# Kernel tuning notes

Hardware: AMD Instinct MI355X
Metric: run time of the kernel (lower is better)

## Reference

```python
import jax, jax.numpy as jnp
import numpy as np

N_LAYERS = 6
N_HEADS = 16
D_EMBED = 1024
D_HEAD = D_EMBED // N_HEADS
VOCAB = 32000
EXP = 4
B, S = 2, 1024


def setup_inputs() -> dict:
    key = jax.random.key(0)
    ks = jax.random.split(key, 24)
    f = jax.random.normal
    inp = {
        "input_ids": jax.random.randint(ks[0], (B, S), 0, VOCAB),
        "encoder_k": f(ks[1], (B, S, D_EMBED), jnp.float32),
        "encoder_v": f(ks[2], (B, S, D_EMBED), jnp.float32),
        "emb": f(ks[3], (VOCAB, D_EMBED), jnp.float32) * 0.02,
        # per-head projection weights (shared across heads), one per layer,
        # for masked self-attn (m) and cross-attn (c). stored as [L, d_head, d_head]
        # applied as x @ W (equivalent param'n of nn.Linear, bias=False)
        "Wq_m": f(ks[4], (N_LAYERS, D_HEAD, D_HEAD), jnp.float32) / np.sqrt(D_HEAD),
        "Wk_m": f(ks[5], (N_LAYERS, D_HEAD, D_HEAD), jnp.float32) / np.sqrt(D_HEAD),
        "Wv_m": f(ks[6], (N_LAYERS, D_HEAD, D_HEAD), jnp.float32) / np.sqrt(D_HEAD),
        "Wq_c": f(ks[7], (N_LAYERS, D_HEAD, D_HEAD), jnp.float32) / np.sqrt(D_HEAD),
        "Wk_c": f(ks[8], (N_LAYERS, D_HEAD, D_HEAD), jnp.float32) / np.sqrt(D_HEAD),
        "Wv_c": f(ks[9], (N_LAYERS, D_HEAD, D_HEAD), jnp.float32) / np.sqrt(D_HEAD),
        "ln1_g": jnp.ones((N_LAYERS, D_EMBED), jnp.float32),
        "ln1_b": jnp.zeros((N_LAYERS, D_EMBED), jnp.float32),
        "ln2_g": jnp.ones((N_LAYERS, D_EMBED), jnp.float32),
        "ln2_b": jnp.zeros((N_LAYERS, D_EMBED), jnp.float32),
        "ln3_g": jnp.ones((N_LAYERS, D_EMBED), jnp.float32),
        "ln3_b": jnp.zeros((N_LAYERS, D_EMBED), jnp.float32),
        "W1": f(ks[10], (N_LAYERS, D_EMBED, EXP * D_EMBED), jnp.float32) / np.sqrt(D_EMBED),
        "b1": jnp.zeros((N_LAYERS, EXP * D_EMBED), jnp.float32),
        "W2": f(ks[11], (N_LAYERS, EXP * D_EMBED, D_EMBED), jnp.float32) / np.sqrt(EXP * D_EMBED),
        "b2": jnp.zeros((N_LAYERS, D_EMBED), jnp.float32),
        "Wout": f(ks[12], (D_EMBED, VOCAB), jnp.float32) / np.sqrt(D_EMBED),
        "bout": jnp.zeros((VOCAB,), jnp.float32),
    }
    return inp


def _layer_norm(x, g, b, eps=1e-5):
    mu = jnp.mean(x, axis=-1, keepdims=True)
    var = jnp.var(x, axis=-1, keepdims=True)
    return (x - mu) * jax.lax.rsqrt(var + eps) * g + b


def _mha(k_in, q_in, v_in, Wk, Wq, Wv, causal_mask):
    b, s, _ = k_in.shape
    # split heads: [b, s, h, d_head]; per-head Linear shared across heads
    k = jnp.einsum("bshd,de->bshe", k_in.reshape(b, s, N_HEADS, D_HEAD), Wk)
    q = jnp.einsum("bshd,de->bshe", q_in.reshape(b, s, N_HEADS, D_HEAD), Wq)
    v = jnp.einsum("bshd,de->bshe", v_in.reshape(b, s, N_HEADS, D_HEAD), Wv)
    scores = jnp.einsum("bqhd,bkhd->bhqk", q, k) / np.sqrt(D_HEAD)
    if causal_mask is not None:
        # quirk of original: masked positions filled with 1e-19 (not -inf)
        scores = jnp.where(causal_mask, scores, jnp.asarray(1e-19, scores.dtype))
    attn = jax.nn.softmax(scores, axis=-1)
    out = jnp.einsum("bhqk,bkhd->bqhd", attn, v)
    return out.reshape(b, s, D_EMBED)


def _pos_encoding(s, d):
    # angle = pos / 10000 ** (2*i / d); sin if i even else cos (faithful quirk)
    pos = jnp.arange(s, dtype=jnp.float32)[:, None]
    i = jnp.arange(d, dtype=jnp.float32)[None, :]
    angle = pos / jnp.power(10000.0, 2.0 * i / d)
    return jnp.where(jnp.arange(d)[None, :] % 2 == 0, jnp.sin(angle), jnp.cos(angle))


def reference(input_ids, encoder_k, encoder_v, emb, Wq_m, Wk_m, Wv_m, Wq_c, Wk_c, Wv_c,
              ln1_g, ln1_b, ln2_g, ln2_b, ln3_g, ln3_b, W1, b1, W2, b2, Wout, bout):
    b, s = input_ids.shape
    causal = jnp.tril(jnp.ones((s, s), bool))[None, None]  # [1,1,s,s]
    x = emb[input_ids] * np.sqrt(D_EMBED) + _pos_encoding(s, D_EMBED)[None]
    for l in range(N_LAYERS):
        op = _mha(x, x, x, Wk_m[l], Wq_m[l], Wv_m[l], causal)
        h1 = _layer_norm(op + x, ln1_g[l], ln1_b[l])
        op = _mha(encoder_k, h1, encoder_v, Wk_c[l], Wq_c[l], Wv_c[l], None)
        h2 = _layer_norm(op + h1, ln2_g[l], ln2_b[l])
        ff = jax.nn.relu(h2 @ W1[l] + b1[l]) @ W2[l] + b2[l]
        x = _layer_norm(ff + h2, ln3_g[l], ln3_b[l])
    return x @ Wout + bout
```

## Files before the change

kernel.cpp:

```cpp
#include <hip/hip_runtime.h>
#include <math.h>

#define NB   2
#define SEQ  1024
#define TOK  2048
#define DEM  1024
#define NH   16
#define DH   64
#define FFD  4096
#define NL   6
#define VOC  32000

typedef __bf16 bf16x8 __attribute__((ext_vector_type(8)));
typedef float  f32x4  __attribute__((ext_vector_type(4)));
typedef const __attribute__((address_space(1))) void gvoid_t;
typedef __attribute__((address_space(3)))       void lvoid_t;

__device__ __forceinline__ int swz8(int r, int c8) {
  return r * 64 + (((c8 >> 3) ^ (r & 7)) << 3);
}

__global__ __launch_bounds__(256) void k_embed(const int* __restrict__ ids,
    const float* __restrict__ emb, float* __restrict__ x)
{
  int t = blockIdx.x;
  int s = t & (SEQ - 1);
  int id = ids[t];
  int d0 = threadIdx.x * 4;
  const float ln10000 = 9.210340371976184f;
  #pragma unroll
  for (int j = 0; j < 4; j++) {
    int i = d0 + j;
    float inv = expf(-(2.0f * (float)i / (float)DEM) * ln10000);
    float ang = (float)s * inv;
    float pe = ((i & 1) == 0) ? sinf(ang) : cosf(ang);
    x[(size_t)t * DEM + i] = emb[(size_t)id * DEM + i] * 32.0f + pe;
  }
}

__global__ __launch_bounds__(256) void k_proj3(
    const float* __restrict__ qi, const float* __restrict__ ki,
    const float* __restrict__ vi,
    const float* __restrict__ Wq, const float* __restrict__ Wk,
    const float* __restrict__ Wv,
    __bf16* __restrict__ qh, __bf16* __restrict__ ql_,
    __bf16* __restrict__ kh, __bf16* __restrict__ kl_,
    __bf16* __restrict__ vt)
{
  __shared__ float Ws[64][64];
  __shared__ float xs[64][68];
  int t0 = blockIdx.x * 64, hh = blockIdx.y, tid = threadIdx.x;
  const float* ins[3]  = {qi, ki, vi};
  const float* Wp[3]   = {Wq, Wk, Wv};
  #pragma unroll 1
  for (int p = 0; p < 3; p++) {
    if (p) __syncthreads();
    #pragma unroll
    for (int i = 0; i < 16; i++) {
      int idx = tid + i * 256;
      int r = idx >> 6, c = idx & 63;
      Ws[r][c] = Wp[p][idx];
      xs[c][r] = ins[p][(size_t)(t0 + r) * DEM + hh * DH + c];
    }
    __syncthreads();
    int e = tid & 63, tq = tid >> 6;
    float acc[16] = {0.f};
    for (int d = 0; d < 64; d++) {
      float w = Ws[d][e];
      float4 x0 = *(float4*)&xs[d][tq * 16 + 0];
      float4 x1 = *(float4*)&xs[d][tq * 16 + 4];
      float4 x2 = *(float4*)&xs[d][tq * 16 + 8];
      float4 x3 = *(float4*)&xs[d][tq * 16 + 12];
      acc[0]  += x0.x * w; acc[1]  += x0.y * w; acc[2]  += x0.z * w; acc[3]  += x0.w * w;
      acc[4]  += x1.x * w; acc[5]  += x1.y * w; acc[6]  += x1.z * w; acc[7]  += x1.w * w;
      acc[8]  += x2.x * w; acc[9]  += x2.y * w; acc[10] += x2.z * w; acc[11] += x2.w * w;
      acc[12] += x3.x * w; acc[13] += x3.y * w; acc[14] += x3.z * w; acc[15] += x3.w * w;
    }
    if (p == 2) {
      alignas(16) __bf16 tmp[16];
      #pragma unroll
      for (int i = 0; i < 16; i++) tmp[i] = (__bf16)acc[i];
      uint4* dst = (uint4*)&vt[(size_t)(hh * DH + e) * TOK + t0 + tq * 16];
      dst[0] = ((uint4*)tmp)[0];
      dst[1] = ((uint4*)tmp)[1];
    } else {
      __bf16* ho = p ? kh : qh;
      __bf16* lo = p ? kl_ : ql_;
      #pragma unroll
      for (int i = 0; i < 16; i++) {
        float v = acc[i];
        __bf16 hv = (__bf16)v;
        size_t idx = (size_t)(t0 + tq * 16 + i) * DEM + hh * DH + e;
        ho[idx] = hv;
        lo[idx] = (__bf16)(v - (float)hv);
      }
    }
  }
}

__global__ __launch_bounds__(256) void k_attn_mfma(
    const __bf16* __restrict__ qh, const __bf16* __restrict__ ql,
    const __bf16* __restrict__ kh, const __bf16* __restrict__ kl,
    const __bf16* __restrict__ vt, float* __restrict__ out, int causal)
{
  __shared__ __bf16 khs[64 * 64];
  __shared__ __bf16 kls[64 * 64];
  __shared__ __bf16 vts[64 * 64];
  __shared__ __bf16 phs[4][16 * 64];
  __shared__ __bf16 pls[4][16 * 64];

  int lin = (blockIdx.z * gridDim.y + blockIdx.y) * gridDim.x + blockIdx.x;
  int lin2 = (lin & 7) * 64 + (lin >> 3);
  int qt = lin2 & 15, h = (lin2 >> 4) & 15, b = lin2 >> 8;

  int tid = threadIdx.x, lane = tid & 63, w = tid >> 6;
  int fr = lane & 15, fkg = lane >> 4;
  int q0 = qt * 64;

  const __bf16* qhb = qh + ((size_t)(b * SEQ + q0 + w * 16 + fr)) * DEM + h * DH;
  const __bf16* qlb = ql + ((size_t)(b * SEQ + q0 + w * 16 + fr)) * DEM + h * DH;
  bf16x8 qf0 = *(const bf16x8*)(qhb + fkg * 8);
  bf16x8 qf1 = *(const bf16x8*)(qhb + fkg * 8 + 32);
  bf16x8 qg0 = *(const bf16x8*)(qlb + fkg * 8);
  bf16x8 qg1 = *(const bf16x8*)(qlb + fkg * 8 + 32);

  const __bf16* khb = kh + ((size_t)b * SEQ) * DEM + h * DH;
  const __bf16* klb = kl + ((size_t)b * SEQ) * DEM + h * DH;
  const __bf16* vtb = vt + (size_t)(h * DH) * TOK + b * SEQ;

  float m[4], l[4] = {0.f, 0.f, 0.f, 0.f};
  m[0] = m[1] = m[2] = m[3] = -INFINITY;
  f32x4 o[4] = {};
  int qrow_g = q0 + w * 16;

  for (int kt = 0; kt < 16; kt++) {
    if (kt) __syncthreads();
    #pragma unroll
    for (int i = 0; i < 2; i++) {
      int cid = tid + i * 256;
      int r = cid >> 3, cc = cid & 7;
      int sc = ((cc ^ (r & 7)) << 3);
      __builtin_amdgcn_global_load_lds(
          (gvoid_t*)(khb + (size_t)(kt * 64 + r) * DEM + sc),
          (lvoid_t*)(khs + cid * 8), 16, 0, 0);
      __builtin_amdgcn_global_load_lds(
          (gvoid_t*)(klb + (size_t)(kt * 64 + r) * DEM + sc),
          (lvoid_t*)(kls + cid * 8), 16, 0, 0);
      __builtin_amdgcn_global_load_lds(
          (gvoid_t*)(vtb + (size_t)r * TOK + kt * 64 + sc),
          (lvoid_t*)(vts + cid * 8), 16, 0, 0);
    }
    __syncthreads();

    f32x4 s[4] = {};
    #pragma unroll
    for (int j = 0; j < 4; j++) {
      int r0 = j * 16 + fr;
      bf16x8 a0 = *(const bf16x8*)(khs + swz8(r0, fkg * 8));
      bf16x8 a1 = *(const bf16x8*)(khs + swz8(r0, fkg * 8 + 32));
      bf16x8 b0 = *(const bf16x8*)(kls + swz8(r0, fkg * 8));
      bf16x8 b1 = *(const bf16x8*)(kls + swz8(r0, fkg * 8 + 32));
      s[j] = __builtin_amdgcn_mfma_f32_16x16x32_bf16(qf0, a0, s[j], 0, 0, 0);
      s[j] = __builtin_amdgcn_mfma_f32_16x16x32_bf16(qf1, a1, s[j], 0, 0, 0);
      s[j] = __builtin_amdgcn_mfma_f32_16x16x32_bf16(qf0, b0, s[j], 0, 0, 0);
      s[j] = __builtin_amdgcn_mfma_f32_16x16x32_bf16(qf1, b1, s[j], 0, 0, 0);
      s[j] = __builtin_amdgcn_mfma_f32_16x16x32_bf16(qg0, a0, s[j], 0, 0, 0);
      s[j] = __builtin_amdgcn_mfma_f32_16x16x32_bf16(qg1, a1, s[j], 0, 0, 0);
    }

    #pragma unroll
    for (int r = 0; r < 4; r++) {
      int qg = qrow_g + fkg * 4 + r;
      float sv[4];
      #pragma unroll
      for (int j = 0; j < 4; j++) {
        float x = s[j][r] * 0.125f;
        int kg = kt * 64 + j * 16 + fr;
        if (causal && kg > qg) x = 1e-19f;
        sv[j] = x;
      }
      float tmax = fmaxf(fmaxf(sv[0], sv[1]), fmaxf(sv[2], sv[3]));
      tmax = fmaxf(tmax, __shfl_xor(tmax, 1));
      tmax = fmaxf(tmax, __shfl_xor(tmax, 2));
      tmax = fmaxf(tmax, __shfl_xor(tmax, 4));
      tmax = fmaxf(tmax, __shfl_xor(tmax, 8));
      float mnew = fmaxf(m[r], tmax);
      float alpha = __expf(m[r] - mnew);
      float p0 = __expf(sv[0] - mnew), p1 = __expf(sv[1] - mnew);
      float p2 = __expf(sv[2] - mnew), p3 = __expf(sv[3] - mnew);
      float rs = p0 + p1 + p2 + p3;
      rs += __shfl_xor(rs, 1); rs += __shfl_xor(rs, 2);
      rs += __shfl_xor(rs, 4); rs += __shfl_xor(rs, 8);
      l[r] = l[r] * alpha + rs;
      m[r] = mnew;
      #pragma unroll
      for (int jd = 0; jd < 4; jd++) o[jd][r] *= alpha;
      int prow = fkg * 4 + r;
      float pv[4] = {p0, p1, p2, p3};
      #pragma unroll
      for (int j = 0; j < 4; j++) {
        int pcol = j * 16 + fr;
        int idx = prow * 64 + (((((pcol >> 3) ^ (prow & 7)) << 3)) | (pcol & 7));
        __bf16 hv = (__bf16)pv[j];
        phs[w][idx] = hv;
        pls[w][idx] = (__bf16)(pv[j] - (float)hv);
      }
    }

    bf16x8 pa0 = *(const bf16x8*)(&phs[w][swz8(fr, fkg * 8)]);
    bf16x8 pa1 = *(const bf16x8*)(&phs[w][swz8(fr, fkg * 8 + 32)]);
    bf16x8 pb0 = *(const bf16x8*)(&pls[w][swz8(fr, fkg * 8)]);
    bf16x8 pb1 = *(const bf16x8*)(&pls[w][swz8(fr, fkg * 8 + 32)]);
    #pragma unroll
    for (int jd = 0; jd < 4; jd++) {
      int vr0 = jd * 16 + fr;
      bf16x8 v0 = *(const bf16x8*)(vts + swz8(vr0, fkg * 8));
      bf16x8 v1 = *(const bf16x8*)(vts + swz8(vr0, fkg * 8 + 32));
      o[jd] = __builtin_amdgcn_mfma_f32_16x16x32_bf16(pa0, v0, o[jd], 0, 0, 0);
      o[jd] = __builtin_amdgcn_mfma_f32_16x16x32_bf16(pa1, v1, o[jd], 0, 0, 0);
      o[jd] = __builtin_amdgcn_mfma_f32_16x16x32_bf16(pb0, v0, o[jd], 0, 0, 0);
      o[jd] = __builtin_amdgcn_mfma_f32_16x16x32_bf16(pb1, v1, o[jd], 0, 0, 0);
    }
  }

  #pragma unroll
  for (int r = 0; r < 4; r++) {
    float inv = 1.0f / l[r];
    size_t row = (size_t)(b * SEQ + q0 + w * 16 + fkg * 4 + r);
    #pragma unroll
    for (int jd = 0; jd < 4; jd++)
      out[row * DEM + h * DH + jd * 16 + fr] = o[jd][r] * inv;
  }
}

__global__ __launch_bounds__(256) void k_addln(const float* __restrict__ a,
    const float* __restrict__ r, const float* __restrict__ g,
    const float* __restrict__ bb, float* __restrict__ out,
    __bf16* __restrict__ obf)
{
  int t = blockIdx.x, tid = threadIdx.x;
  size_t base = (size_t)t * DEM + tid * 4;
  float4 av = *(const float4*)&a[base];
  float4 rv = *(const float4*)&r[base];
  float x0 = av.x + rv.x, x1 = av.y + rv.y, x2 = av.z + rv.z, x3 = av.w + rv.w;
  float s = x0 + x1 + x2 + x3;
  float qq = x0 * x0 + x1 * x1 + x2 * x2 + x3 * x3;
  #pragma unroll
  for (int msk = 32; msk; msk >>= 1) {
    s  += __shfl_xor(s, msk);
    qq += __shfl_xor(qq, msk);
  }
  __shared__ float red[8];
  if ((tid & 63) == 0) { red[tid >> 6] = s; red[4 + (tid >> 6)] = qq; }
  __syncthreads();
  s  = red[0] + red[1] + red[2] + red[3];
  qq = red[4] + red[5] + red[6] + red[7];
  float mu = s * (1.0f / DEM);
  float var = qq * (1.0f / DEM) - mu * mu;
  float rstd = rsqrtf(var + 1e-5f);
  float4 gv = *(const float4*)&g[tid * 4];
  float4 bv = *(const float4*)&bb[tid * 4];
  float4 ov;
  ov.x = (x0 - mu) * rstd * gv.x + bv.x;
  ov.y = (x1 - mu) * rstd * gv.y + bv.y;
  ov.z = (x2 - mu) * rstd * gv.z + bv.z;
  ov.w = (x3 - mu) * rstd * gv.w + bv.w;
  *(float4*)&out[base] = ov;
  if (obf) {
    __bf16 tb[4] = {(__bf16)ov.x, (__bf16)ov.y, (__bf16)ov.z, (__bf16)ov.w};
    *(uint2*)&obf[base] = *(uint2*)tb;
  }
}

__global__ __launch_bounds__(256) void k_cvt_t(const float* __restrict__ W,
    __bf16* __restrict__ Wt, int K, int N)
{
  __shared__ float t[64][65];
  int n0 = blockIdx.x * 64, k0 = blockIdx.y * 64;
  int tid = threadIdx.x;
  int c = (tid & 15) * 4, r = tid >> 4;
  #pragma unroll
  for (int i = 0; i < 4; i++) {
    float4 v = *(const float4*)&W[(size_t)(k0 + r + i * 16) * N + n0 + c];
    t[r + i * 16][c] = v.x; t[r + i * 16][c + 1] = v.y;
    t[r + i * 16][c + 2] = v.z; t[r + i * 16][c + 3] = v.w;
  }
  __syncthreads();
  int row = tid >> 2, ko = (tid & 3) * 16;
  alignas(16) __bf16 tmp[16];
  #pragma unroll
  for (int j = 0; j < 16; j++) tmp[j] = (__bf16)t[ko + j][row];
  uint4* dst = (uint4*)&Wt[(size_t)(n0 + row) * K + k0 + ko];
  dst[0] = ((uint4*)tmp)[0];
  dst[1] = ((uint4*)tmp)[1];
}

template <int OUT_BF, int RELU>
__global__ __launch_bounds__(256) void k_gemm_bf(
    const __bf16* __restrict__ A, const __bf16* __restrict__ Bt,
    const float* __restrict__ bias, void* __restrict__ Cout,
    int M, int N, int K)
{
  __shared__ __bf16 As[128 * 32];
  __shared__ __bf16 Bs[128 * 32];
  int tid = threadIdx.x;
  int gx = gridDim.x;
  int nwg = gx * gridDim.y;
  int lin = blockIdx.y * gx + blockIdx.x;
  if ((nwg & 7) == 0) {
    int cpx = nwg >> 3;
    lin = (lin & 7) * cpx + (lin >> 3);
  }
  int m0 = (lin % gx) * 128, n0 = (lin / gx) * 128;
  const __bf16* Ab = A + (size_t)m0 * K;
  const __bf16* Bb = Bt + (size_t)n0 * K;
  int lane = tid & 63, wave = tid >> 6;
  int wm = (wave >> 1) * 64, wn = (wave & 1) * 64;
  int fr = lane & 15;
  int fk = (lane >> 4) * 8;
  f32x4 acc[4][4] = {};

  const __bf16* Ald = As + (wm + fr) * 32 + fk;
  const __bf16* Bld = Bs + (wn + fr) * 32 + fk;

  for (int kt = 0; kt < K; kt += 32) {
    __syncthreads();
    #pragma unroll
    for (int i = 0; i < 2; i++) {
      int idx = tid + i * 256;
      int row = idx >> 2, ko = (idx & 3) * 8;
      __builtin_amdgcn_global_load_lds(
          (gvoid_t*)(Ab + (size_t)row * K + kt + ko),
          (lvoid_t*)(As + idx * 8), 16, 0, 0);
      __builtin_amdgcn_global_load_lds(
          (gvoid_t*)(Bb + (size_t)row * K + kt + ko),
          (lvoid_t*)(Bs + idx * 8), 16, 0, 0);
    }
    __syncthreads();
    bf16x8 af[4], bfr[4];
    #pragma unroll
    for (int i = 0; i < 4; i++) af[i]  = *(const bf16x8*)(Ald + i * 16 * 32);
    #pragma unroll
    for (int j = 0; j < 4; j++) bfr[j] = *(const bf16x8*)(Bld + j * 16 * 32);
    #pragma unroll
    for (int i = 0; i < 4; i++)
      #pragma unroll
      for (int j = 0; j < 4; j++)
        acc[i][j] = __builtin_amdgcn_mfma_f32_16x16x32_bf16(
            af[i], bfr[j], acc[i][j], 0, 0, 0);
  }
  int orow = (lane >> 4) * 4, ocol = lane & 15;
  #pragma unroll
  for (int i = 0; i < 4; i++) {
    #pragma unroll
    for (int j = 0; j < 4; j++) {
      int col = n0 + wn + j * 16 + ocol;
      float bsv = bias[col];
      #pragma unroll
      for (int r = 0; r < 4; r++) {
        size_t row = (size_t)(m0 + wm + i * 16 + orow + r);
        float u = acc[i][j][r] + bsv;
        if (RELU) u = fmaxf(u, 0.f);
        if (OUT_BF) ((__bf16*)Cout)[row * N + col] = (__bf16)u;
        else        ((float*)Cout)[row * N + col] = u;
      }
    }
  }
}

extern "C" void kernel_launch(void* const* d_in, const int* in_sizes, int n_in,
                              void* d_out, int out_size, void* d_ws, size_t ws_size,
                              hipStream_t stream) {
  const int*   ids   = (const int*)  d_in[0];
  const float* enc_k = (const float*)d_in[1];
  const float* enc_v = (const float*)d_in[2];
  const float* emb   = (const float*)d_in[3];
  const float* Wq_m  = (const float*)d_in[4];
  const float* Wk_m  = (const float*)d_in[5];
  const float* Wv_m  = (const float*)d_in[6];
  const float* Wq_c  = (const float*)d_in[7];
  const float* Wk_c  = (const float*)d_in[8];
  const float* Wv_c  = (const float*)d_in[9];
  const float* ln1_g = (const float*)d_in[10];
  const float* ln1_b = (const float*)d_in[11];
  const float* ln2_g = (const float*)d_in[12];
  const float* ln2_b = (const float*)d_in[13];
  const float* ln3_g = (const float*)d_in[14];
  const float* ln3_b = (const float*)d_in[15];
  const float* W1    = (const float*)d_in[16];
  const float* b1    = (const float*)d_in[17];
  const float* W2    = (const float*)d_in[18];
  const float* b2    = (const float*)d_in[19];
  const float* Wout  = (const float*)d_in[20];
  const float* bout  = (const float*)d_in[21];
  float* out = (float*)d_out;

  const size_t TD = (size_t)TOK * DEM;
  float* ws = (float*)d_ws;
  float* x  = ws;
  float* h  = ws + TD;
  float* op = ws + 2 * TD;
  float* qb = ws + 3 * TD;
  float* kb = ws + 4 * TD;
  float* vb = ws + 5 * TD;
  __bf16* ffb   = (__bf16*)qb;
  __bf16* abf   = (__bf16*)(ws + 6 * TD);
  __bf16* w1t   = abf + TD;
  __bf16* w2t   = w1t + (size_t)FFD * DEM;
  __bf16* woutt = w2t + (size_t)FFD * DEM;

  __bf16* qhb = (__bf16*)qb;  __bf16* qlb = qhb + TD;
  __bf16* khb = (__bf16*)kb;  __bf16* klb = khb + TD;
  __bf16* vtb = (__bf16*)vb;

  dim3 blk(256);
  dim3 gproj(TOK / 64, NH);
  dim3 gattn(SEQ / 64, NH, NB);

  k_embed<<<TOK, blk, 0, stream>>>(ids, emb, x);
  k_cvt_t<<<dim3(VOC / 64, DEM / 64), blk, 0, stream>>>(Wout, woutt, DEM, VOC);

  for (int l = 0; l < NL; l++) {
    const size_t wofs = (size_t)l * DH * DH;
    const size_t lofs = (size_t)l * DEM;
    k_proj3<<<gproj, blk, 0, stream>>>(x, x, x,
        Wq_m + wofs, Wk_m + wofs, Wv_m + wofs, qhb, qlb, khb, klb, vtb);
    k_attn_mfma<<<gattn, blk, 0, stream>>>(qhb, qlb, khb, klb, vtb, op, 1);
    k_addln<<<TOK, blk, 0, stream>>>(op, x, ln1_g + lofs, ln1_b + lofs, h, nullptr);
    k_proj3<<<gproj, blk, 0, stream>>>(h, enc_k, enc_v,
        Wq_c + wofs, Wk_c + wofs, Wv_c + wofs, qhb, qlb, khb, klb, vtb);
    k_attn_mfma<<<gattn, blk, 0, stream>>>(qhb, qlb, khb, klb, vtb, op, 0);
    k_addln<<<TOK, blk, 0, stream>>>(op, h, ln2_g + lofs, ln2_b + lofs, h, abf);
    k_cvt_t<<<dim3(FFD / 64, DEM / 64), blk, 0, stream>>>(
        W1 + (size_t)l * DEM * FFD, w1t, DEM, FFD);
    k_cvt_t<<<dim3(DEM / 64, FFD / 64), blk, 0, stream>>>(
        W2 + (size_t)l * FFD * DEM, w2t, FFD, DEM);
    k_gemm_bf<1, 1><<<dim3(TOK / 128, FFD / 128), blk, 0, stream>>>(
        abf, w1t, b1 + (size_t)l * FFD, (void*)ffb, TOK, FFD, DEM);
    k_gemm_bf<0, 0><<<dim3(TOK / 128, DEM / 128), blk, 0, stream>>>(
        ffb, w2t, b2 + lofs, (void*)op, TOK, DEM, FFD);
    k_addln<<<TOK, blk, 0, stream>>>(op, h, ln3_g + lofs, ln3_b + lofs, x, abf);
  }
  k_gemm_bf<0, 0><<<dim3(TOK / 128, VOC / 128), blk, 0, stream>>>(
      abf, woutt, bout, (void*)out, TOK, VOC, DEM);
}
```

Before: 2.778 ms.

## Double-buffer K/V tiles in attention and drop P low-part MFMAs

Double-buffers the K-high, K-low and V tiles in LDS so the next tile's global-to-LDS loads are issued before the current tile is computed, using explicit vmcnt waits and raw barriers in place of syncthreads. It also removes the bf16 residual (low part) of the softmax probabilities, halving the P·V MFMA count and LDS traffic, and raises wave priority around the MFMA sections. Keeping only the high bf16 part of P lowers accuracy of the attention output. Double-buffering increases LDS usage per block, which may reduce occupancy.

```diff
diff --git a/kernel.cpp b/kernel.cpp
--- a/kernel.cpp
+++ b/kernel.cpp
@@ -103,11 +103,10 @@
     const __bf16* __restrict__ kh, const __bf16* __restrict__ kl,
     const __bf16* __restrict__ vt, float* __restrict__ out, int causal)
 {
-  __shared__ __bf16 khs[64 * 64];
-  __shared__ __bf16 kls[64 * 64];
-  __shared__ __bf16 vts[64 * 64];
+  __shared__ __bf16 khs[2][64 * 64];
+  __shared__ __bf16 kls[2][64 * 64];
+  __shared__ __bf16 vts[2][64 * 64];
   __shared__ __bf16 phs[4][16 * 64];
-  __shared__ __bf16 pls[4][16 * 64];
 
   int lin = (blockIdx.z * gridDim.y + blockIdx.y) * gridDim.x + blockIdx.x;
   int lin2 = (lin & 7) * 64 + (lin >> 3);
@@ -128,13 +127,7 @@
   const __bf16* klb = kl + ((size_t)b * SEQ) * DEM + h * DH;
   const __bf16* vtb = vt + (size_t)(h * DH) * TOK + b * SEQ;
 
-  float m[4], l[4] = {0.f, 0.f, 0.f, 0.f};
-  m[0] = m[1] = m[2] = m[3] = -INFINITY;
-  f32x4 o[4] = {};
-  int qrow_g = q0 + w * 16;
-
-  for (int kt = 0; kt < 16; kt++) {
-    if (kt) __syncthreads();
+  auto STAGE = [&](int buf, int kt) {
     #pragma unroll
     for (int i = 0; i < 2; i++) {
       int cid = tid + i * 256;
@@ -142,24 +135,42 @@
       int sc = ((cc ^ (r & 7)) << 3);
       __builtin_amdgcn_global_load_lds(
           (gvoid_t*)(khb + (size_t)(kt * 64 + r) * DEM + sc),
-          (lvoid_t*)(khs + cid * 8), 16, 0, 0);
+          (lvoid_t*)(&khs[buf][cid * 8]), 16, 0, 0);
       __builtin_amdgcn_global_load_lds(
           (gvoid_t*)(klb + (size_t)(kt * 64 + r) * DEM + sc),
-          (lvoid_t*)(kls + cid * 8), 16, 0, 0);
+          (lvoid_t*)(&kls[buf][cid * 8]), 16, 0, 0);
       __builtin_amdgcn_global_load_lds(
           (gvoid_t*)(vtb + (size_t)r * TOK + kt * 64 + sc),
-          (lvoid_t*)(vts + cid * 8), 16, 0, 0);
-    }
-    __syncthreads();
+          (lvoid_t*)(&vts[buf][cid * 8]), 16, 0, 0);
+    }
+  };
+
+  float m[4], l[4] = {0.f, 0.f, 0.f, 0.f};
+  m[0] = m[1] = m[2] = m[3] = -INFINITY;
+  f32x4 o[4] = {};
+  int qrow_g = q0 + w * 16;
+
+  STAGE(0, 0);
+
+  for (int kt = 0; kt < 16; kt++) {
+    int cur = kt & 1;
+    if (kt < 15) {
+      STAGE(cur ^ 1, kt + 1);
+      asm volatile("s_waitcnt vmcnt(6)" ::: "memory");
+    } else {
+      asm volatile("s_waitcnt vmcnt(0)" ::: "memory");
+    }
+    __builtin_amdgcn_s_barrier();
 
     f32x4 s[4] = {};
+    __builtin_amdgcn_s_setprio(1);
     #pragma unroll
     for (int j = 0; j < 4; j++) {
       int r0 = j * 16 + fr;
-      bf16x8 a0 = *(const bf16x8*)(khs + swz8(r0, fkg * 8));
-      bf16x8 a1 = *(const bf16x8*)(khs + swz8(r0, fkg * 8 + 32));
-      bf16x8 b0 = *(const bf16x8*)(kls + swz8(r0, fkg * 8));
-      bf16x8 b1 = *(const bf16x8*)(kls + swz8(r0, fkg * 8 + 32));
+      bf16x8 a0 = *(const bf16x8*)(&khs[cur][swz8(r0, fkg * 8)]);
+      bf16x8 a1 = *(const bf16x8*)(&khs[cur][swz8(r0, fkg * 8 + 32)]);
+      bf16x8 b0 = *(const bf16x8*)(&kls[cur][swz8(r0, fkg * 8)]);
+      bf16x8 b1 = *(const bf16x8*)(&kls[cur][swz8(r0, fkg * 8 + 32)]);
       s[j] = __builtin_amdgcn_mfma_f32_16x16x32_bf16(qf0, a0, s[j], 0, 0, 0);
       s[j] = __builtin_amdgcn_mfma_f32_16x16x32_bf16(qf1, a1, s[j], 0, 0, 0);
       s[j] = __builtin_amdgcn_mfma_f32_16x16x32_bf16(qf0, b0, s[j], 0, 0, 0);
@@ -167,6 +178,7 @@
       s[j] = __builtin_amdgcn_mfma_f32_16x16x32_bf16(qg0, a0, s[j], 0, 0, 0);
       s[j] = __builtin_amdgcn_mfma_f32_16x16x32_bf16(qg1, a1, s[j], 0, 0, 0);
     }
+    __builtin_amdgcn_s_setprio(0);
 
     #pragma unroll
     for (int r = 0; r < 4; r++) {
@@ -201,26 +213,23 @@
       for (int j = 0; j < 4; j++) {
         int pcol = j * 16 + fr;
         int idx = prow * 64 + (((((pcol >> 3) ^ (prow & 7)) << 3)) | (pcol & 7));
-        __bf16 hv = (__bf16)pv[j];
-        phs[w][idx] = hv;
-        pls[w][idx] = (__bf16)(pv[j] - (float)hv);
+        phs[w][idx] = (__bf16)pv[j];
       }
     }
 
     bf16x8 pa0 = *(const bf16x8*)(&phs[w][swz8(fr, fkg * 8)]);
     bf16x8 pa1 = *(const bf16x8*)(&phs[w][swz8(fr, fkg * 8 + 32)]);
-    bf16x8 pb0 = *(const bf16x8*)(&pls[w][swz8(fr, fkg * 8)]);
-    bf16x8 pb1 = *(const bf16x8*)(&pls[w][swz8(fr, fkg * 8 + 32)]);
+    __builtin_amdgcn_s_setprio(1);
     #pragma unroll
     for (int jd = 0; jd < 4; jd++) {
       int vr0 = jd * 16 + fr;
-      bf16x8 v0 = *(const bf16x8*)(vts + swz8(vr0, fkg * 8));
-      bf16x8 v1 = *(const bf16x8*)(vts + swz8(vr0, fkg * 8 + 32));
+      bf16x8 v0 = *(const bf16x8*)(&vts[cur][swz8(vr0, fkg * 8)]);
+      bf16x8 v1 = *(const bf16x8*)(&vts[cur][swz8(vr0, fkg * 8 + 32)]);
       o[jd] = __builtin_amdgcn_mfma_f32_16x16x32_bf16(pa0, v0, o[jd], 0, 0, 0);
       o[jd] = __builtin_amdgcn_mfma_f32_16x16x32_bf16(pa1, v1, o[jd], 0, 0, 0);
-      o[jd] = __builtin_amdgcn_mfma_f32_16x16x32_bf16(pb0, v0, o[jd], 0, 0, 0);
-      o[jd] = __builtin_amdgcn_mfma_f32_16x16x32_bf16(pb1, v1, o[jd], 0, 0, 0);
-    }
+    }
+    __builtin_amdgcn_s_setprio(0);
+    __builtin_amdgcn_s_barrier();
   }
 
   #pragma unroll
```

Result: faster. 2.722 ms (-2.0%).
